# Performance work log

Measured on AMD Instinct MI355X. Metric: run time of the kernel, lower is better.

The kernel has to match this reference:

```python
import jax, jax.numpy as jnp
import numpy as np

N = 100000
E = 1600000
D_IN, H1, H2 = 64, 128, 64
ATT = 32


def _mean_aggregate(feat, src, dst, num_nodes):
    # gather source features per edge, scatter-sum to destinations, divide by in-degree
    summed = jax.ops.segment_sum(feat[src], dst, num_segments=num_nodes)  # [N, d]
    deg = jax.ops.segment_sum(jnp.ones((src.shape[0],), feat.dtype), dst, num_segments=num_nodes)
    return summed / jnp.maximum(deg, 1.0)[:, None]


def setup_inputs() -> dict:
    key = jax.random.key(0)
    ks = jax.random.split(key, 16)
    x = jax.random.normal(ks[0], (N, D_IN), dtype=jnp.float32)
    edge_index = jax.random.randint(ks[1], (2, E), 0, N, dtype=jnp.int64)

    def lin(k, fan_in, fan_out):
        bound = 1.0 / np.sqrt(fan_in)
        return jax.random.uniform(k, (fan_in, fan_out), jnp.float32, -bound, bound)

    params = {
        'W1_l': lin(ks[2], D_IN, H1), 'W1_r': lin(ks[3], D_IN, H1),
        'b1': jnp.zeros((H1,), jnp.float32),
        'W2_l': lin(ks[4], H1, H2), 'W2_r': lin(ks[5], H1, H2),
        'b2': jnp.zeros((H2,), jnp.float32),
        'Wa': lin(ks[6], H2, ATT), 'ba': jnp.zeros((ATT,), jnp.float32),
        'ctx': jax.random.normal(ks[7], (ATT,), jnp.float32),
        'Wc1': lin(ks[8], H2, H2 // 2), 'bc1': jnp.zeros((H2 // 2,), jnp.float32),
        'Wc2': lin(ks[9], H2 // 2, 1), 'bc2': jnp.zeros((1,), jnp.float32),
    }
    return {'x': x, 'edge_index': edge_index, **params}


def reference(x, edge_index, W1_l, W1_r, b1, W2_l, W2_r, b2, Wa, ba, ctx, Wc1, bc1, Wc2, bc2):
    src, dst = edge_index[0], edge_index[1]
    ionm_alerts = x[:, -1]  # [N]

    # GraphSAGE layer 1 (mean aggr): lin_l(mean_neighbors) + lin_r(x_self)
    agg1 = _mean_aggregate(x, src, dst, N)
    h = jax.nn.relu(agg1 @ W1_l + b1 + x @ W1_r)  # [N, H1]
    # F.dropout(training=False) -> identity

    # GraphSAGE layer 2
    agg2 = _mean_aggregate(h, src, dst, N)
    h = jax.nn.relu(agg2 @ W2_l + b2 + h @ W2_r)  # [N, H2]

    # attention with IONM alert boost (+0.4)
    scores = jnp.tanh(h @ Wa + ba)            # [N, ATT]
    w = scores @ ctx + ionm_alerts * 0.4       # [N]
    w = jax.nn.softmax(w, axis=0)
    h = h * w[:, None]

    pooled = jnp.mean(h, axis=0, keepdims=True)  # [1, H2]

    # classifier head (Dropout identity in eval)
    z = jax.nn.relu(pooled @ Wc1 + bc1)
    return jax.nn.sigmoid(z @ Wc2 + bc2)  # [1, 1]
```

## Files before the change

### kernel.cpp

```cpp
#include <hip/hip_runtime.h>
#include <math.h>

#define N_NODES 100000
#define E_EDGES 1600000
#define D_IN 64
#define HID1 128
#define HID2 64
#define ATT 32
#define CAP 32
#define AT_STRIDE 136
#define NRANGE 8
#define RNODES (N_NODES / NRANGE)
#define NPART 64
#define XCAST_BLOCKS ((N_NODES * 16 + 255) / 256)
#define SCAT_BLOCKS 2048

typedef unsigned int uint32;
typedef unsigned short ushort;
typedef __attribute__((ext_vector_type(8))) short short8;
typedef __attribute__((ext_vector_type(4))) float float4v;

#define NTL(p) __builtin_nontemporal_load(&(p))

__device__ inline uint32 bf16rn(float f){ uint32 u = __float_as_uint(f); return (u + 0x7fffu + ((u >> 16) & 1u)) >> 16; }
__device__ inline uint32 packbf2(float a, float b){ return bf16rn(a) | (bf16rn(b) << 16); }

#if __has_builtin(__builtin_amdgcn_cvt_f32_fp8) && __has_builtin(__builtin_amdgcn_cvt_pk_fp8_f32)
#define HW_FP8 1
#endif

__device__ inline uint32 fp8_enc_sw(float f){
    float a = fabsf(f);
    uint32 s = (__float_as_uint(f) >> 24) & 0x80u;
    if (!(a >= 0.001953125f)) return s;
    if (a > 448.f) return s | 0x7Eu;
    if (a < 0.015625f){
        uint32 c = (uint32)rintf(a * 512.f);
        return s | c;
    }
    int e; float m = frexpf(a, &e);
    int E = e - 1;
    float mant = 2.f * m;
    uint32 mc = (uint32)rintf((mant - 1.f) * 8.f);
    uint32 Ec = (uint32)(E + 7);
    if (mc == 8u){ mc = 0u; Ec += 1u; }
    if (Ec >= 16u || (Ec == 15u && mc > 6u)) return s | 0x7Eu;
    return s | (Ec << 3) | mc;
}

__device__ inline float fp8_dec_sw(uint32 c){
    uint32 s = (c & 0x80u) << 24;
    uint32 E = (c >> 3) & 0xFu, m = c & 7u;
    float v;
    if (E == 0) v = (float)m * 0.001953125f;
    else v = __uint_as_float(((E + 120u) << 23) | (m << 20));
    return __uint_as_float(__float_as_uint(v) | s);
}

__device__ inline uint32 enc4(float a, float b, float c, float d){
#ifdef HW_FP8
    int r = __builtin_amdgcn_cvt_pk_fp8_f32(a, b, 0, false);
    r = __builtin_amdgcn_cvt_pk_fp8_f32(c, d, r, true);
    return (uint32)r;
#else
    return fp8_enc_sw(a) | (fp8_enc_sw(b) << 8) | (fp8_enc_sw(c) << 16) | (fp8_enc_sw(d) << 24);
#endif
}

__device__ inline void dec4acc(uint32 w, float& a0, float& a1, float& a2, float& a3){
#ifdef HW_FP8
    a0 += __builtin_amdgcn_cvt_f32_fp8((int)w, 0);
    a1 += __builtin_amdgcn_cvt_f32_fp8((int)w, 1);
    a2 += __builtin_amdgcn_cvt_f32_fp8((int)w, 2);
    a3 += __builtin_amdgcn_cvt_f32_fp8((int)w, 3);
#else
    a0 += fp8_dec_sw(w & 0xffu);
    a1 += fp8_dec_sw((w >> 8) & 0xffu);
    a2 += fp8_dec_sw((w >> 16) & 0xffu);
    a3 += fp8_dec_sw(w >> 24);
#endif
}

__global__ void k_mega(const float* __restrict__ x,
                       const int* __restrict__ src, const int* __restrict__ dst,
                       const float* __restrict__ W1l, const float* __restrict__ W1r,
                       const float* __restrict__ W2l, const float* __restrict__ W2r,
                       uint32* __restrict__ xb, uint32* __restrict__ xq,
                       uint32* __restrict__ vq,
                       ushort* __restrict__ wt1g, ushort* __restrict__ wt2g,
                       int* __restrict__ cnt, int* __restrict__ ssrc){
    int b = blockIdx.x, t = threadIdx.x;
    if (b < XCAST_BLOCKS){
        int i = b * 256 + t;
        if (i < N_NODES * 16){
            float4v v = NTL(((const float4v*)x)[i]);
            xb[2 * i]     = packbf2(v.x, v.y);
            xb[2 * i + 1] = packbf2(v.z, v.w);
            xq[i] = enc4(v.x, v.y, v.z, v.w);
        }
        return;
    }
    if (b < XCAST_BLOCKS + 2){
        int sub = b - XCAST_BLOCKS;
        ushort* dstp = (sub == 0) ? wt1g : wt2g;
        for (int idx = t; idx < 128 * 128; idx += 256){
            int nn = idx >> 7, kk = idx & 127;
            float v;
            if (sub == 0) v = (kk < 64) ? W1l[kk * 128 + nn] : W1r[(kk - 64) * 128 + nn];
            else          v = (nn < 64) ? W2l[kk * 64 + nn]  : W2r[kk * 64 + (nn - 64)];
            dstp[nn * 128 + kk] = (ushort)bf16rn(v);
        }
        if (sub == 0){
            if (t < 16) xq[(size_t)N_NODES * 16 + t] = 0u;
            else if (t < 32) vq[(size_t)N_NODES * 16 + (t - 16)] = 0u;
        }
        return;
    }
    int rel = b - (XCAST_BLOCKS + 2);
    int range = rel & (NRANGE - 1);
    int blk   = rel >> 3;
    int lo = range * RNODES, hi = lo + RNODES;
    const int stride = (SCAT_BLOCKS / NRANGE) * 256;
    int i0 = blk * 256 + t;
    #pragma unroll 1
    for (int base = 0; base < 32; base += 8){
        int d[8], sv[8], pos[8];
        bool inr[8];
        #pragma unroll
        for (int u = 0; u < 8; u++){
            int i = i0 + (base + u) * stride;
            d[u] = (i < E_EDGES) ? NTL(dst[i]) : -1;
        }
        #pragma unroll
        for (int u = 0; u < 8; u++)
            inr[u] = (d[u] >= lo) && (d[u] < hi);
        #pragma unroll
        for (int u = 0; u < 8; u++){
            int i = i0 + (base + u) * stride;
            if (inr[u]) sv[u] = NTL(src[i]);
        }
        #pragma unroll
        for (int u = 0; u < 8; u++){
            if (inr[u]) pos[u] = atomicAdd(&cnt[d[u]], 1);
        }
        #pragma unroll
        for (int u = 0; u < 8; u++){
            if (inr[u] && pos[u] < CAP) ssrc[d[u] * CAP + pos[u]] = sv[u];
        }
    }
}

__device__ inline void gather8_fp8(const uint32* __restrict__ tab,
                                   const int* __restrict__ ssrc,
                                   const int* __restrict__ cnt,
                                   int n0, int lane,
                                   float acc[8][4], int cct[8]){
    int q = lane >> 4, p = lane & 15;
    int nn = n0 + (lane & 7);
    int ccl_ = cnt[nn];
    int cc[8];
    #pragma unroll
    for (int j = 0; j < 8; j++){
        int c = __shfl(ccl_, j, 64);
        cct[j] = c;
        cc[j] = min(c, CAP);
    }
    #pragma unroll
    for (int j = 0; j < 8; j++){ acc[j][0] = acc[j][1] = acc[j][2] = acc[j][3] = 0.f; }
    int cmax = 0;
    #pragma unroll
    for (int j = 0; j < 8; j++) cmax = max(cmax, cc[j]);
    if (cmax == 0) return;
    int se[8];
    #pragma unroll
    for (int j = 0; j < 8; j++)
        se[j] = (lane < cc[j]) ? NTL(ssrc[(n0 + j) * CAP + lane]) : N_NODES;
    int iters = (cmax + 3) >> 2;
    uint32 w0[8], w1[8];
    #pragma unroll
    for (int j = 0; j < 8; j++){
        int s = __shfl(se[j], q, 64);
        w0[j] = tab[(uint32)s * 16u + p];
    }
    {
        int idx1 = (iters > 1) ? (4 + q) : q;
        #pragma unroll
        for (int j = 0; j < 8; j++){
            int s = __shfl(se[j], idx1, 64);
            w1[j] = tab[(uint32)s * 16u + p];
        }
    }
    for (int it = 0; it < iters; it++){
        uint32 w2[8];
        bool m2 = (it + 2 < iters);
        if (m2){
            int idx = (it + 2) * 4 + q;
            #pragma unroll
            for (int j = 0; j < 8; j++){
                int s = __shfl(se[j], idx, 64);
                w2[j] = tab[(uint32)s * 16u + p];
            }
        }
        #pragma unroll
        for (int j = 0; j < 8; j++)
            dec4acc(w0[j], acc[j][0], acc[j][1], acc[j][2], acc[j][3]);
        #pragma unroll
        for (int j = 0; j < 8; j++) w0[j] = w1[j];
        if (m2){
            #pragma unroll
            for (int j = 0; j < 8; j++) w1[j] = w2[j];
        }
    }
    #pragma unroll
    for (int j = 0; j < 8; j++){
        acc[j][0] += __shfl_xor(acc[j][0], 16, 64); acc[j][1] += __shfl_xor(acc[j][1], 16, 64);
        acc[j][2] += __shfl_xor(acc[j][2], 16, 64); acc[j][3] += __shfl_xor(acc[j][3], 16, 64);
        acc[j][0] += __shfl_xor(acc[j][0], 32, 64); acc[j][1] += __shfl_xor(acc[j][1], 32, 64);
        acc[j][2] += __shfl_xor(acc[j][2], 32, 64); acc[j][3] += __shfl_xor(acc[j][3], 32, 64);
    }
}

__device__ inline float inv_deg(int c){ return 1.f / fmaxf(fminf((float)c, (float)CAP), 1.f); }

__global__ __launch_bounds__(256) void k_layer1(
    const uint32* __restrict__ xq, const uint32* __restrict__ xb,
    const int* __restrict__ ssrc, const int* __restrict__ cnt,
    const ushort* __restrict__ wt1g, const ushort* __restrict__ wt2g,
    const float* __restrict__ b1, const float* __restrict__ b2,
    uint32* __restrict__ vq, float* __restrict__ r2f,
    float* __restrict__ pzero){
    __shared__ ushort smem[2 * 32 * AT_STRIDE];
    ushort* at  = smem;
    ushort* at2 = smem + 32 * AT_STRIDE;
    float* vstage = (float*)smem;
    int t = threadIdx.x, wave = t >> 6, lane = t & 63;
    if (blockIdx.x == 0){
        for (int i = t; i < NPART * 65; i += 256) pzero[i] = 0.f;
    }
    int nb0 = blockIdx.x * 32;
    int n0 = nb0 + wave * 8;

    int m0 = t >> 3, ch = t & 7;
    uint4 xval = *(const uint4*)&xb[(size_t)(nb0 + m0) * 32 + ch * 4];

    float acc[8][4]; int cct[8];
    gather8_fp8(xq, ssrc, cnt, n0, lane, acc, cct);
    int p = lane & 15;
    if (lane < 16){
        #pragma unroll
        for (int j = 0; j < 8; j++){
            float inv = inv_deg(cct[j]);
            uint2 o;
            o.x = packbf2(acc[j][0] * inv, acc[j][1] * inv);
            o.y = packbf2(acc[j][2] * inv, acc[j][3] * inv);
            *(uint2*)&at[(wave * 8 + j) * AT_STRIDE + 4 * p] = o;
        }
    }
    *(uint4*)((uint32*)(at + m0 * AT_STRIDE + 64) + ch * 4) = xval;
    __syncthreads();

    int cidx = lane & 15, quad = lane >> 4;
    int mt = wave >> 1;
    int nbase = (wave & 1) * 64;
    float4v c[4];
    #pragma unroll
    for (int nt = 0; nt < 4; nt++) c[nt] = (float4v){0.f,0.f,0.f,0.f};
    #pragma unroll
    for (int kt = 0; kt < 4; kt++){
        short8 a = *(short8*)(at + ((mt * 16 + cidx) * AT_STRIDE + kt * 32 + quad * 8));
        #pragma unroll
        for (int nt = 0; nt < 4; nt++){
            short8 b = *(const short8*)(wt1g + ((nbase + nt * 16 + cidx) * 128 + kt * 32 + quad * 8));
            c[nt] = __builtin_amdgcn_mfma_f32_16x16x32_bf16(a, b, c[nt], 0, 0, 0);
        }
    }
    #pragma unroll
    for (int nt = 0; nt < 4; nt++){
        float bb = b1[nbase + nt * 16 + cidx];
        #pragma unroll
        for (int i = 0; i < 4; i++){
            int row = quad * 4 + i;
            at2[(mt * 16 + row) * AT_STRIDE + nbase + nt * 16 + cidx] =
                (ushort)bf16rn(fmaxf(c[nt][i] + bb, 0.f));
        }
    }
    __syncthreads();
    #pragma unroll
    for (int nt = 0; nt < 4; nt++) c[nt] = (float4v){0.f,0.f,0.f,0.f};
    #pragma unroll
    for (int kt = 0; kt < 4; kt++){
        short8 a = *(short8*)(at2 + ((mt * 16 + cidx) * AT_STRIDE + kt * 32 + quad * 8));
        #pragma unroll
        for (int nt = 0; nt < 4; nt++){
            short8 b = *(const short8*)(wt2g + ((nbase + nt * 16 + cidx) * 128 + kt * 32 + quad * 8));
            c[nt] = __builtin_amdgcn_mfma_f32_16x16x32_bf16(a, b, c[nt], 0, 0, 0);
        }
    }
    if (nbase == 0){
        #pragma unroll
        for (int nt = 0; nt < 4; nt++){
            #pragma unroll
            for (int i = 0; i < 4; i++){
                int row = quad * 4 + i;
                vstage[(mt * 16 + row) * 65 + nt * 16 + cidx] = c[nt][i];
            }
        }
    } else {
        #pragma unroll
        for (int nt = 0; nt < 4; nt++){
            float bb = b2[nt * 16 + cidx];
            #pragma unroll
            for (int i = 0; i < 4; i++){
                int row = quad * 4 + i;
                size_t node = nb0 + mt * 16 + row;
                r2f[node * 64 + nt * 16 + cidx] = c[nt][i] + bb;
            }
        }
    }
    __syncthreads();
    {
        int m = t >> 3, u = t & 7;
        float f0 = vstage[m * 65 + 8 * u],     f1 = vstage[m * 65 + 8 * u + 1];
        float f2 = vstage[m * 65 + 8 * u + 2], f3 = vstage[m * 65 + 8 * u + 3];
        float f4 = vstage[m * 65 + 8 * u + 4], f5 = vstage[m * 65 + 8 * u + 5];
        float f6 = vstage[m * 65 + 8 * u + 6], f7 = vstage[m * 65 + 8 * u + 7];
        vq[(size_t)(nb0 + m) * 16 + 2 * u]     = enc4(f0, f1, f2, f3);
        vq[(size_t)(nb0 + m) * 16 + 2 * u + 1] = enc4(f4, f5, f6, f7);
    }
}

__global__ __launch_bounds__(256) void k_gather2f(
    const float* __restrict__ x, const uint32* __restrict__ vq,
    const int* __restrict__ ssrc, const int* __restrict__ cnt,
    const float* __restrict__ r2f,
    const float* __restrict__ Wa, const float* __restrict__ ba, const float* __restrict__ ctx,
    float* __restrict__ pooledP, float* __restrict__ Zpart){
    __shared__ float sh2[32][68];
    __shared__ float sew[32];
    __shared__ float sp[4][64];
    int t = threadIdx.x, wave = t >> 6, lane = t & 63;
    int bn0 = blockIdx.x * 32;
    int n0 = bn0 + wave * 8;
    float acc[8][4]; int cct[8];
    gather8_fp8(vq, ssrc, cnt, n0, lane, acc, cct);
    int p = lane & 15;
    if (lane < 16){
        #pragma unroll
        for (int j = 0; j < 8; j++){
            size_t nj = n0 + j;
            float inv = inv_deg(cct[j]);
            float4v rr = NTL(*(const float4v*)&r2f[nj * 64 + 4 * p]);
            float4v hv;
            hv.x = fmaxf(acc[j][0] * inv + rr.x, 0.f);
            hv.y = fmaxf(acc[j][1] * inv + rr.y, 0.f);
            hv.z = fmaxf(acc[j][2] * inv + rr.z, 0.f);
            hv.w = fmaxf(acc[j][3] * inv + rr.w, 0.f);
            *(float4v*)&sh2[wave * 8 + j][4 * p] = hv;
        }
    }
    __syncthreads();
    int node = t >> 3;
    int c0 = (t & 7) * 4;
    float s0 = ba[c0], s1 = ba[c0 + 1], s2 = ba[c0 + 2], s3 = ba[c0 + 3];
    #pragma unroll 8
    for (int j = 0; j < 64; j++){
        float hv = sh2[node][j];
        s0 += hv * Wa[j * ATT + c0];
        s1 += hv * Wa[j * ATT + c0 + 1];
        s2 += hv * Wa[j * ATT + c0 + 2];
        s3 += hv * Wa[j * ATT + c0 + 3];
    }
    float pa = tanhf(s0) * ctx[c0] + tanhf(s1) * ctx[c0 + 1]
             + tanhf(s2) * ctx[c0 + 2] + tanhf(s3) * ctx[c0 + 3];
    #pragma unroll
    for (int off = 4; off >= 1; off >>= 1) pa += __shfl_down(pa, off, 8);
    if ((t & 7) == 0){
        int n = bn0 + node;
        float w = pa + NTL(x[(size_t)n * 64 + 63]) * 0.4f;
        sew[node] = expf(w);
    }
    __syncthreads();
    int j = t & 63, q = t >> 6;
    float p4 = 0.f;
    #pragma unroll
    for (int m = 0; m < 8; m++) p4 += sh2[q * 8 + m][j] * sew[q * 8 + m];
    sp[q][j] = p4;
    __syncthreads();
    if (t < 64){
        float s = sp[0][t] + sp[1][t] + sp[2][t] + sp[3][t];
        atomicAdd(&pooledP[(blockIdx.x & (NPART - 1)) * 64 + t], s);
    }
    if (t == 64){
        float z = 0.f;
        #pragma unroll
        for (int m = 0; m < 32; m++) z += sew[m];
        atomicAdd(&Zpart[blockIdx.x & (NPART - 1)], z);
    }
}

__global__ void k_final(const float* __restrict__ pooledP, const float* __restrict__ Zpart,
                        const float* __restrict__ Wc1, const float* __restrict__ bc1,
                        const float* __restrict__ Wc2, const float* __restrict__ bc2,
                        float* __restrict__ out){
    __shared__ float sp[64], sz[32];
    __shared__ float Zs;
    int t = threadIdx.x;
    float s = 0.f;
    for (int q = 0; q < NPART; q++) s += pooledP[q * 64 + t];
    if (t == 0){
        float z = 0.f;
        for (int q = 0; q < NPART; q++) z += Zpart[q];
        Zs = z;
    }
    __syncthreads();
    float scale = 1.0f / (Zs * (float)N_NODES);
    sp[t] = s * scale;
    __syncthreads();
    if (t < 32){
        float a = bc1[t];
        #pragma unroll 8
        for (int j = 0; j < 64; j++) a += sp[j] * Wc1[j * 32 + t];
        sz[t] = fmaxf(a, 0.f);
    }
    __syncthreads();
    if (t == 0){
        float a = bc2[0];
        #pragma unroll
        for (int i = 0; i < 32; i++) a += sz[i] * Wc2[i];
        out[0] = 1.0f / (1.0f + expf(-a));
    }
}

extern "C" void kernel_launch(void* const* d_in, const int* in_sizes, int n_in,
                              void* d_out, int out_size, void* d_ws, size_t ws_size,
                              hipStream_t stream) {
    const float* x   = (const float*)d_in[0];
    const int*   ei  = (const int*)d_in[1];
    const int*   src = ei;
    const int*   dst = ei + E_EDGES;
    const float* W1l = (const float*)d_in[2];
    const float* W1r = (const float*)d_in[3];
    const float* b1  = (const float*)d_in[4];
    const float* W2l = (const float*)d_in[5];
    const float* W2r = (const float*)d_in[6];
    const float* b2  = (const float*)d_in[7];
    const float* Wa  = (const float*)d_in[8];
    const float* ba  = (const float*)d_in[9];
    const float* ctx = (const float*)d_in[10];
    const float* Wc1 = (const float*)d_in[11];
    const float* bc1 = (const float*)d_in[12];
    const float* Wc2 = (const float*)d_in[13];
    const float* bc2 = (const float*)d_in[14];

    char* p = (char*)d_ws;
    int* cnt    = (int*)p;                 p += (size_t)N_NODES * 4;
    int* ssrc   = (int*)p;                 p += (size_t)N_NODES * CAP * 4;
    uint32* xb  = (uint32*)p;              p += (size_t)N_NODES * 32 * 4;
    uint32* xq  = (uint32*)p;              p += (size_t)(N_NODES + 1) * 16 * 4;
    uint32* vq  = (uint32*)p;              p += (size_t)(N_NODES + 1) * 16 * 4;
    float* r2f  = (float*)p;               p += (size_t)N_NODES * 64 * 4;
    ushort* wt1g = (ushort*)p;             p += 128 * 128 * 2;
    ushort* wt2g = (ushort*)p;             p += 128 * 128 * 2;
    float* pooledP = (float*)p;            p += NPART * 64 * 4;
    float* Zpart   = (float*)p;            p += NPART * 4;

    hipMemsetAsync(cnt, 0, (size_t)N_NODES * 4, stream);

    k_mega<<<XCAST_BLOCKS + 2 + SCAT_BLOCKS, 256, 0, stream>>>(
        x, src, dst, W1l, W1r, W2l, W2r, xb, xq, vq, wt1g, wt2g, cnt, ssrc);

    k_layer1<<<(N_NODES + 31) / 32, 256, 0, stream>>>(xq, xb, ssrc, cnt,
                                                      wt1g, wt2g, b1, b2, vq, r2f, pooledP);
    k_gather2f<<<(N_NODES + 31) / 32, 256, 0, stream>>>(x, vq, ssrc, cnt, r2f,
                                                        Wa, ba, ctx, pooledP, Zpart);
    k_final<<<1, 64, 0, stream>>>(pooledP, Zpart, Wc1, bc1, Wc2, bc2, (float*)d_out);
}
```

Baseline: 314.3 us.

## Two-pass edge scatter: bucket edges by destination range, then scatter per range

```diff
diff --git a/kernel.cpp b/kernel.cpp
--- a/kernel.cpp
+++ b/kernel.cpp
@@ -13,12 +13,16 @@
 #define RNODES (N_NODES / NRANGE)
 #define NPART 64
 #define XCAST_BLOCKS ((N_NODES * 16 + 255) / 256)
-#define SCAT_BLOCKS 2048
+#define NBLK 1024
+#define EPB  1563
+#define SEGCAP 384
+#define SCAT2_BLOCKS 2048
 
 typedef unsigned int uint32;
 typedef unsigned short ushort;
 typedef __attribute__((ext_vector_type(8))) short short8;
 typedef __attribute__((ext_vector_type(4))) float float4v;
+typedef __attribute__((ext_vector_type(2))) unsigned int uint32x2;
 
 #define NTL(p) __builtin_nontemporal_load(&(p))
 
@@ -88,7 +92,7 @@
                        uint32* __restrict__ xb, uint32* __restrict__ xq,
                        uint32* __restrict__ vq,
                        ushort* __restrict__ wt1g, ushort* __restrict__ wt2g,
-                       int* __restrict__ cnt, int* __restrict__ ssrc){
+                       uint32x2* __restrict__ qu, int* __restrict__ qlen){
     int b = blockIdx.x, t = threadIdx.x;
     if (b < XCAST_BLOCKS){
         int i = b * 256 + t;
@@ -116,36 +120,64 @@
         }
         return;
     }
-    int rel = b - (XCAST_BLOCKS + 2);
-    int range = rel & (NRANGE - 1);
-    int blk   = rel >> 3;
-    int lo = range * RNODES, hi = lo + RNODES;
-    const int stride = (SCAT_BLOCKS / NRANGE) * 256;
-    int i0 = blk * 256 + t;
+    int blk = b - (XCAST_BLOCKS + 2);
+    __shared__ int tails[NRANGE];
+    if (t < NRANGE) tails[t] = 0;
+    __syncthreads();
+    int lane = t & 63;
+    int base = blk * EPB;
+    int end  = min(base + EPB, E_EDGES);
+    for (int i0 = base; i0 < end; i0 += 256){
+        int i = i0 + t;
+        bool v = (i < end);
+        int d = 0, s = 0, r = NRANGE;
+        if (v){
+            d = NTL(dst[i]);
+            s = NTL(src[i]);
+            r = (int)((uint32)d / (uint32)RNODES);
+        }
+        int mybase = 0, myoff = 0;
+        #pragma unroll
+        for (int k = 0; k < NRANGE; k++){
+            unsigned long long mk = __ballot(r == k);
+            if (r == k){
+                int leader = (int)__ffsll((unsigned long long)mk) - 1;
+                int nk = (int)__popcll(mk);
+                int bse = 0;
+                if (lane == leader) bse = atomicAdd(&tails[k], nk);
+                bse = __shfl(bse, leader, 64);
+                mybase = bse;
+                myoff  = (int)__popcll(mk & ((lane == 63) ? 0x7fffffffffffffffull
+                                                          : ((1ull << lane) - 1ull)));
+            }
+        }
+        if (v){
+            int pos = mybase + myoff;
+            if (pos < SEGCAP)
+                qu[(size_t)(blk * NRANGE + r) * SEGCAP + pos] = (uint32x2){(uint32)d, (uint32)s};
+        }
+    }
+    __syncthreads();
+    if (t < NRANGE) qlen[blk * NRANGE + t] = min(tails[t], SEGCAP);
+}
+
+__global__ __launch_bounds__(256) void k_scat2(const uint32x2* __restrict__ qu,
+                                               const int* __restrict__ qlen,
+                                               int* __restrict__ cnt, int* __restrict__ ssrc){
+    int bb = blockIdx.x, t = threadIdx.x;
+    int r = bb & (NRANGE - 1);
+    int sidx = bb >> 3;
     #pragma unroll 1
-    for (int base = 0; base < 32; base += 8){
-        int d[8], sv[8], pos[8];
-        bool inr[8];
-        #pragma unroll
-        for (int u = 0; u < 8; u++){
-            int i = i0 + (base + u) * stride;
-            d[u] = (i < E_EDGES) ? NTL(dst[i]) : -1;
-        }
-        #pragma unroll
-        for (int u = 0; u < 8; u++)
-            inr[u] = (d[u] >= lo) && (d[u] < hi);
-        #pragma unroll
-        for (int u = 0; u < 8; u++){
-            int i = i0 + (base + u) * stride;
-            if (inr[u]) sv[u] = NTL(src[i]);
-        }
-        #pragma unroll
-        for (int u = 0; u < 8; u++){
-            if (inr[u]) pos[u] = atomicAdd(&cnt[d[u]], 1);
-        }
-        #pragma unroll
-        for (int u = 0; u < 8; u++){
-            if (inr[u] && pos[u] < CAP) ssrc[d[u] * CAP + pos[u]] = sv[u];
+    for (int k = 0; k < NBLK / (SCAT2_BLOCKS / NRANGE); k++){
+        int seg = sidx * 4 + k;
+        int qi = seg * NRANGE + r;
+        int len = min(qlen[qi], SEGCAP);
+        const uint32x2* qp = &qu[(size_t)qi * SEGCAP];
+        for (int i = t; i < len; i += 256){
+            uint32x2 pr = NTL(qp[i]);
+            int d = (int)pr.x, s = (int)pr.y;
+            int pos = atomicAdd(&cnt[d], 1);
+            if (pos < CAP) ssrc[d * CAP + pos] = s;
         }
     }
 }
@@ -463,11 +495,15 @@
     ushort* wt2g = (ushort*)p;             p += 128 * 128 * 2;
     float* pooledP = (float*)p;            p += NPART * 64 * 4;
     float* Zpart   = (float*)p;            p += NPART * 4;
+    int* qlen      = (int*)p;              p += (size_t)NBLK * NRANGE * 4;
+    uint32x2* qu = (uint32x2*)r2f;
 
     hipMemsetAsync(cnt, 0, (size_t)N_NODES * 4, stream);
 
-    k_mega<<<XCAST_BLOCKS + 2 + SCAT_BLOCKS, 256, 0, stream>>>(
-        x, src, dst, W1l, W1r, W2l, W2r, xb, xq, vq, wt1g, wt2g, cnt, ssrc);
+    k_mega<<<XCAST_BLOCKS + 2 + NBLK, 256, 0, stream>>>(
+        x, src, dst, W1l, W1r, W2l, W2r, xb, xq, vq, wt1g, wt2g, qu, qlen);
+
+    k_scat2<<<SCAT2_BLOCKS, 256, 0, stream>>>(qu, qlen, cnt, ssrc);
 
     k_layer1<<<(N_NODES + 31) / 32, 256, 0, stream>>>(xq, xb, ssrc, cnt,
                                                       wt1g, wt2g, b1, b2, vq, r2f, pooledP);
```

Result: slower. 322.7 us (+2.7%).
